# Kernel tuning notes

Measured on AMD Instinct MI355X. Metric: run time of the kernel, lower is better.

The kernel has to match this reference:

```python
import jax, jax.numpy as jnp
import numpy as np

N_NODES = 50000


def gcn_conv(x, W, b, src, dst, n):
    """PyG-style GCNConv: symmetric-normalized aggregation over A + I.
    x: [N, Fin], W: [Fin, Fout], b: [Fout], src/dst: [E] int edge endpoints.
    """
    h = x @ W  # [N, Fout]
    # degree with self-loops: deg[i] = 1 + in-degree(i)
    deg = jnp.zeros((n,), dtype=h.dtype).at[dst].add(1.0) + 1.0
    dinv = jax.lax.rsqrt(deg)  # deg^-1/2
    norm_e = dinv[src] * dinv[dst]  # [E]
    # message passing: sum_j norm_ij * h_j  (plus self-loop term deg_i^-1 * h_i)
    agg = jnp.zeros_like(h).at[dst].add(h[src] * norm_e[:, None])
    agg = agg + h * (dinv * dinv)[:, None]
    return agg + b


def setup_inputs() -> dict:
    key = jax.random.key(0)
    ks = jax.random.split(key, 9)
    N, F_in, H, C = N_NODES, 128, 64, 4
    E = 1600000
    node_features = jax.random.normal(ks[0], (N, F_in), dtype=jnp.float32)
    edge_index = jax.random.randint(ks[1], (2, E), 0, N, dtype=jnp.int32)
    s1 = 1.0 / np.sqrt(F_in)
    s2 = 1.0 / np.sqrt(H)
    W1 = jax.random.uniform(ks[2], (F_in, H), jnp.float32, -s1, s1)
    b1 = jax.random.uniform(ks[3], (H,), jnp.float32, -s1, s1)
    W2 = jax.random.uniform(ks[4], (H, H), jnp.float32, -s2, s2)
    b2 = jax.random.uniform(ks[5], (H,), jnp.float32, -s2, s2)
    W3 = jax.random.uniform(ks[6], (H, C), jnp.float32, -s2, s2)
    b3 = jax.random.uniform(ks[7], (C,), jnp.float32, -s2, s2)
    return {"node_features": node_features, "edge_index": edge_index,
            "W1": W1, "b1": b1, "W2": W2, "b2": b2, "W3": W3, "b3": b3}


def reference(node_features, edge_index, W1, b1, W2, b2, W3, b3):
    n = node_features.shape[0]
    src, dst = edge_index[0], edge_index[1]
    out = jax.nn.relu(gcn_conv(node_features, W1, b1, src, dst, n))
    # layer2 applied 7 times with SHARED weights (faithful to the source)
    for _ in range(7):
        out = jax.nn.relu(gcn_conv(out, W2, b2, src, dst, n))
    out = gcn_conv(out, W3, b3, src, dst, n)
    return jax.nn.softmax(out, axis=0)  # softmax over the node dimension (dim=0)
```

## Files before the change

kernel.cpp:

```cpp
#include <hip/hip_runtime.h>
#include <hip/hip_fp16.h>
#include <math.h>
#include <float.h>



__global__ __launch_bounds__(256) void k_count(const int* __restrict__ dst,
                                               unsigned* __restrict__ deg, int E) {
    int e = blockIdx.x * 256 + threadIdx.x;
    if (e < E) atomicAdd(&deg[dst[e]], 1u);
}

__global__ __launch_bounds__(256) void k_dinv(const unsigned* __restrict__ deg,
                                              float* __restrict__ dinv, int n) {
    int i = blockIdx.x * 256 + threadIdx.x;
    if (i < n) dinv[i] = rsqrtf(1.0f + (float)deg[i]);
}

__global__ __launch_bounds__(256) void k_scan1(const unsigned* __restrict__ deg,
                                               int* __restrict__ row_start,
                                               unsigned* __restrict__ bsum, int n) {
    __shared__ unsigned t[256];
    int i = blockIdx.x * 256 + threadIdx.x;
    unsigned v = (i < n) ? deg[i] : 0u;
    t[threadIdx.x] = v;
    __syncthreads();
    #pragma unroll
    for (int off = 1; off < 256; off <<= 1) {
        unsigned u = (threadIdx.x >= (unsigned)off) ? t[threadIdx.x - off] : 0u;
        __syncthreads();
        t[threadIdx.x] += u;
        __syncthreads();
    }
    if (i < n) row_start[i] = (int)(t[threadIdx.x] - v);
    if (threadIdx.x == 255) bsum[blockIdx.x] = t[255];
}

__global__ __launch_bounds__(256) void k_scan2(unsigned* __restrict__ bsum,
                                               int* __restrict__ row_start,
                                               int nb, int n) {
    __shared__ unsigned t[256];
    unsigned v = (threadIdx.x < (unsigned)nb) ? bsum[threadIdx.x] : 0u;
    t[threadIdx.x] = v;
    __syncthreads();
    #pragma unroll
    for (int off = 1; off < 256; off <<= 1) {
        unsigned u = (threadIdx.x >= (unsigned)off) ? t[threadIdx.x - off] : 0u;
        __syncthreads();
        t[threadIdx.x] += u;
        __syncthreads();
    }
    if (threadIdx.x < (unsigned)nb) bsum[threadIdx.x] = t[threadIdx.x] - v;
    if (threadIdx.x == 255) row_start[n] = (int)t[255];
}

__global__ __launch_bounds__(256) void k_scan3(int* __restrict__ row_start,
                                               const unsigned* __restrict__ bsum, int n) {
    int i = blockIdx.x * 256 + threadIdx.x;
    if (i < n) row_start[i] += (int)bsum[blockIdx.x];
}

__global__ __launch_bounds__(256) void k_fill(const int* __restrict__ src,
                                              const int* __restrict__ dst,
                                              const int* __restrict__ row_start,
                                              unsigned* __restrict__ cursor,
                                              int* __restrict__ csr_src, int E) {
    int e = blockIdx.x * 256 + threadIdx.x;
    if (e >= E) return;
    int s = src[e], d = dst[e];
    unsigned pos = atomicAdd(&cursor[d], 1u);
    csr_src[row_start[d] + (int)pos] = s;
}


__global__ __launch_bounds__(256) void k_gemm64_f32(const float* __restrict__ x,
                                                    const float* __restrict__ W,
                                                    const float* __restrict__ dinv,
                                                    __half* __restrict__ hs, int n) {
    __shared__ float Wl[128 * 64];
    for (int idx = threadIdx.x; idx < 128 * 64; idx += 256) Wl[idx] = W[idx];
    __syncthreads();
    int wave = threadIdx.x >> 6, lane = threadIdx.x & 63;
    int base = blockIdx.x * 64 + wave * 16;
    for (int it = 0; it < 16; ++it) {
        int i = base + it;
        if (i < n) {
            const float4* xr = (const float4*)(x + (size_t)i * 128);
            float acc = 0.f;
            #pragma unroll
            for (int k4 = 0; k4 < 32; ++k4) {
                float4 v = xr[k4];
                acc += v.x * Wl[(k4 * 4 + 0) * 64 + lane];
                acc += v.y * Wl[(k4 * 4 + 1) * 64 + lane];
                acc += v.z * Wl[(k4 * 4 + 2) * 64 + lane];
                acc += v.w * Wl[(k4 * 4 + 3) * 64 + lane];
            }
            hs[(size_t)i * 64 + lane] = __float2half(acc * dinv[i]);
        }
    }
}


__global__ __launch_bounds__(256) void k_gemm64_f16(const __half* __restrict__ xh,
                                                    const float* __restrict__ W,
                                                    const float* __restrict__ dinv,
                                                    __half* __restrict__ hs, int n) {
    __shared__ float Wl[64 * 64];
    for (int idx = threadIdx.x; idx < 64 * 64; idx += 256) Wl[idx] = W[idx];
    __syncthreads();
    int wave = threadIdx.x >> 6, lane = threadIdx.x & 63;
    int base = blockIdx.x * 64 + wave * 16;
    for (int it = 0; it < 16; ++it) {
        int i = base + it;
        if (i < n) {
            const __half2* xr = (const __half2*)(xh + (size_t)i * 64);
            float acc = 0.f;
            #pragma unroll
            for (int k2 = 0; k2 < 32; ++k2) {
                float2 v = __half22float2(xr[k2]);
                acc += v.x * Wl[(k2 * 2 + 0) * 64 + lane];
                acc += v.y * Wl[(k2 * 2 + 1) * 64 + lane];
            }
            hs[(size_t)i * 64 + lane] = __float2half(acc * dinv[i]);
        }
    }
}

__global__ __launch_bounds__(256) void k_gemm4(const __half* __restrict__ xh,
                                               const float* __restrict__ W,
                                               const float* __restrict__ dinv,
                                               float4* __restrict__ h4, int n) {
    __shared__ float Wl[256];
    for (int idx = threadIdx.x; idx < 256; idx += 256) Wl[idx] = W[idx];
    __syncthreads();
    int i = blockIdx.x * 256 + threadIdx.x;
    if (i >= n) return;
    const __half2* ar = (const __half2*)(xh + (size_t)i * 64);
    float a0 = 0.f, a1 = 0.f, a2 = 0.f, a3 = 0.f;
    #pragma unroll
    for (int k2 = 0; k2 < 32; ++k2) {
        float2 v = __half22float2(ar[k2]);
        int k = k2 * 2;
        a0 += v.x * Wl[k * 4 + 0] + v.y * Wl[(k + 1) * 4 + 0];
        a1 += v.x * Wl[k * 4 + 1] + v.y * Wl[(k + 1) * 4 + 1];
        a2 += v.x * Wl[k * 4 + 2] + v.y * Wl[(k + 1) * 4 + 2];
        a3 += v.x * Wl[k * 4 + 3] + v.y * Wl[(k + 1) * 4 + 3];
    }
    float di = dinv[i];
    h4[i] = make_float4(a0 * di, a1 * di, a2 * di, a3 * di);
}


__global__ __launch_bounds__(256) void k_agg64h(const __half* __restrict__ hs,
                                                const float* __restrict__ dinv,
                                                const int* __restrict__ row_start,
                                                const int* __restrict__ csr_src,
                                                const float* __restrict__ bias,
                                                __half* __restrict__ out, int n) {
    int gw = (int)((blockIdx.x * 256 + threadIdx.x) >> 6);
    int lane = threadIdx.x & 63;
    if (gw >= n) return;
    float acc = __half2float(hs[(size_t)gw * 64 + lane]);
    int s = row_start[gw], e = row_start[gw + 1];
    int slot = s;
    for (; slot + 8 <= e; slot += 8) {
        int i0 = csr_src[slot + 0], i1 = csr_src[slot + 1];
        int i2 = csr_src[slot + 2], i3 = csr_src[slot + 3];
        int i4 = csr_src[slot + 4], i5 = csr_src[slot + 5];
        int i6 = csr_src[slot + 6], i7 = csr_src[slot + 7];
        float v0 = __half2float(hs[(size_t)i0 * 64 + lane]);
        float v1 = __half2float(hs[(size_t)i1 * 64 + lane]);
        float v2 = __half2float(hs[(size_t)i2 * 64 + lane]);
        float v3 = __half2float(hs[(size_t)i3 * 64 + lane]);
        float v4 = __half2float(hs[(size_t)i4 * 64 + lane]);
        float v5 = __half2float(hs[(size_t)i5 * 64 + lane]);
        float v6 = __half2float(hs[(size_t)i6 * 64 + lane]);
        float v7 = __half2float(hs[(size_t)i7 * 64 + lane]);
        acc += ((v0 + v1) + (v2 + v3)) + ((v4 + v5) + (v6 + v7));
    }
    for (; slot < e; ++slot)
        acc += __half2float(hs[(size_t)csr_src[slot] * 64 + lane]);
    acc = acc * dinv[gw] + bias[lane];
    out[(size_t)gw * 64 + lane] = __float2half(fmaxf(acc, 0.f));
}


__global__ __launch_bounds__(256) void k_agg4(const float4* __restrict__ h4,
                                              const float* __restrict__ dinv,
                                              const int* __restrict__ row_start,
                                              const int* __restrict__ csr_src,
                                              const float* __restrict__ b3,
                                              float4* __restrict__ z, int n) {
    int i = blockIdx.x * 256 + threadIdx.x;
    if (i >= n) return;
    float4 self = h4[i];
    float a0 = self.x, a1 = self.y, a2 = self.z, a3 = self.w;
    int s = row_start[i], e = row_start[i + 1];
    int slot = s;
    for (; slot + 4 <= e; slot += 4) {
        int s0 = csr_src[slot], s1 = csr_src[slot + 1];
        int s2 = csr_src[slot + 2], s3 = csr_src[slot + 3];
        float4 v0 = h4[s0], v1 = h4[s1], v2 = h4[s2], v3 = h4[s3];
        a0 += v0.x + v1.x + v2.x + v3.x;
        a1 += v0.y + v1.y + v2.y + v3.y;
        a2 += v0.z + v1.z + v2.z + v3.z;
        a3 += v0.w + v1.w + v2.w + v3.w;
    }
    for (; slot < e; ++slot) {
        float4 v = h4[csr_src[slot]];
        a0 += v.x; a1 += v.y; a2 += v.z; a3 += v.w;
    }
    float di = dinv[i];
    z[i] = make_float4(a0 * di + b3[0], a1 * di + b3[1],
                       a2 * di + b3[2], a3 * di + b3[3]);
}


__device__ inline unsigned encf(float f) {
    unsigned u = __float_as_uint(f);
    return (u & 0x80000000u) ? ~u : (u | 0x80000000u);
}
__device__ inline float decf(unsigned e) {
    return (e & 0x80000000u) ? __uint_as_float(e & 0x7FFFFFFFu) : __uint_as_float(~e);
}

__global__ __launch_bounds__(256) void k_max(const float4* __restrict__ z,
                                             unsigned* __restrict__ gmax, int n) {
    float m0 = -FLT_MAX, m1 = -FLT_MAX, m2 = -FLT_MAX, m3 = -FLT_MAX;
    for (int i = blockIdx.x * 256 + threadIdx.x; i < n; i += gridDim.x * 256) {
        float4 v = z[i];
        m0 = fmaxf(m0, v.x); m1 = fmaxf(m1, v.y);
        m2 = fmaxf(m2, v.z); m3 = fmaxf(m3, v.w);
    }
    #pragma unroll
    for (int off = 32; off; off >>= 1) {
        m0 = fmaxf(m0, __shfl_xor(m0, off));
        m1 = fmaxf(m1, __shfl_xor(m1, off));
        m2 = fmaxf(m2, __shfl_xor(m2, off));
        m3 = fmaxf(m3, __shfl_xor(m3, off));
    }
    if ((threadIdx.x & 63) == 0) {
        atomicMax(&gmax[0], encf(m0));
        atomicMax(&gmax[1], encf(m1));
        atomicMax(&gmax[2], encf(m2));
        atomicMax(&gmax[3], encf(m3));
    }
}

__global__ __launch_bounds__(256) void k_exp(const float4* __restrict__ z,
                                             float4* __restrict__ out,
                                             const unsigned* __restrict__ gmax,
                                             float* __restrict__ gsum, int n) {
    float M0 = decf(gmax[0]), M1 = decf(gmax[1]), M2 = decf(gmax[2]), M3 = decf(gmax[3]);
    float s0 = 0.f, s1 = 0.f, s2 = 0.f, s3 = 0.f;
    for (int i = blockIdx.x * 256 + threadIdx.x; i < n; i += gridDim.x * 256) {
        float4 v = z[i];
        float4 e;
        e.x = expf(v.x - M0); e.y = expf(v.y - M1);
        e.z = expf(v.z - M2); e.w = expf(v.w - M3);
        out[i] = e;
        s0 += e.x; s1 += e.y; s2 += e.z; s3 += e.w;
    }
    #pragma unroll
    for (int off = 32; off; off >>= 1) {
        s0 += __shfl_xor(s0, off);
        s1 += __shfl_xor(s1, off);
        s2 += __shfl_xor(s2, off);
        s3 += __shfl_xor(s3, off);
    }
    if ((threadIdx.x & 63) == 0) {
        atomicAdd(&gsum[0], s0);
        atomicAdd(&gsum[1], s1);
        atomicAdd(&gsum[2], s2);
        atomicAdd(&gsum[3], s3);
    }
}

__global__ __launch_bounds__(256) void k_norm(float4* __restrict__ out,
                                              const float* __restrict__ gsum, int n) {
    float r0 = 1.f / gsum[0], r1 = 1.f / gsum[1], r2 = 1.f / gsum[2], r3 = 1.f / gsum[3];
    for (int i = blockIdx.x * 256 + threadIdx.x; i < n; i += gridDim.x * 256) {
        float4 v = out[i];
        v.x *= r0; v.y *= r1; v.z *= r2; v.w *= r3;
        out[i] = v;
    }
}


extern "C" void kernel_launch(void* const* d_in, const int* in_sizes, int n_in,
                              void* d_out, int out_size, void* d_ws, size_t ws_size,
                              hipStream_t stream) {
    const float* x0 = (const float*)d_in[0];
    const int* ei = (const int*)d_in[1];
    const float* W1 = (const float*)d_in[2];
    const float* b1 = (const float*)d_in[3];
    const float* W2 = (const float*)d_in[4];
    const float* b2 = (const float*)d_in[5];
    const float* W3 = (const float*)d_in[6];
    const float* b3 = (const float*)d_in[7];

    const int n = in_sizes[0] / 128;
    const int E = in_sizes[1] / 2;
    const int* src = ei;
    const int* dst = ei + E;

    char* ws = (char*)d_ws;
    size_t off = 0;
    auto alloc = [&](size_t bytes) -> void* {
        void* p = (void*)(ws + off);
        off = (off + bytes + 255) & ~(size_t)255;
        return p;
    };

    unsigned* deg    = (unsigned*)alloc((size_t)n * 4);
    unsigned* cursor = (unsigned*)alloc((size_t)n * 4);
    unsigned* gmax   = (unsigned*)alloc(16);
    float*    gsum   = (float*)alloc(16);
    size_t zero_bytes = off;

    float* dinv      = (float*)alloc((size_t)n * 4);
    int*   row_start = (int*)alloc((size_t)(n + 1) * 4);
    unsigned* bsum   = (unsigned*)alloc(1024 * 4);
    int*   csr_src   = (int*)alloc((size_t)E * 4);
    __half* hbuf     = (__half*)alloc((size_t)n * 64 * 2);
    __half* xbuf     = (__half*)alloc((size_t)n * 64 * 2);
    float4* h4buf    = (float4*)alloc((size_t)n * 16);
    float4* zbuf     = (float4*)alloc((size_t)n * 16);

    hipMemsetAsync(deg, 0, zero_bytes, stream);

    const int nbE = (E + 255) / 256;
    const int nbN = (n + 255) / 256;

    k_count<<<nbE, 256, 0, stream>>>(dst, deg, E);
    k_dinv<<<nbN, 256, 0, stream>>>(deg, dinv, n);
    k_scan1<<<nbN, 256, 0, stream>>>(deg, row_start, bsum, n);
    k_scan2<<<1, 256, 0, stream>>>(bsum, row_start, nbN, n);
    k_scan3<<<nbN, 256, 0, stream>>>(row_start, bsum, n);
    k_fill<<<nbE, 256, 0, stream>>>(src, dst, row_start, cursor, csr_src, E);

    const int nbG = (n + 63) / 64;
    const int nbA = (n * 64 + 255) / 256;

    k_gemm64_f32<<<nbG, 256, 0, stream>>>(x0, W1, dinv, hbuf, n);
    k_agg64h<<<nbA, 256, 0, stream>>>(hbuf, dinv, row_start, csr_src, b1, xbuf, n);

    for (int l = 0; l < 7; ++l) {
        k_gemm64_f16<<<nbG, 256, 0, stream>>>(xbuf, W2, dinv, hbuf, n);
        k_agg64h<<<nbA, 256, 0, stream>>>(hbuf, dinv, row_start, csr_src, b2, xbuf, n);
    }

    k_gemm4<<<nbN, 256, 0, stream>>>(xbuf, W3, dinv, h4buf, n);
    k_agg4<<<nbN, 256, 0, stream>>>(h4buf, dinv, row_start, csr_src, b3, zbuf, n);

    k_max<<<256, 256, 0, stream>>>(zbuf, gmax, n);
    k_exp<<<256, 256, 0, stream>>>(zbuf, (float4*)d_out, gmax, gsum, n);
    k_norm<<<256, 256, 0, stream>>>((float4*)d_out, gsum, n);
}
```

Before: 985.8 us.

## Partition CSR count/fill atomics by destination range and widen aggregation unroll

The degree-count and CSR-fill kernels now launch a fixed grid of 8 partitions times 104 blocks. Each block strides over all edges but only does atomics for destinations in its partition's node range, and blockIdx low bits pick the partition. The intent is to keep each partition's atomics in a narrower address range, likely to localise them per XCD/L2 and cut cross-die atomic traffic, at the cost of every partition re-reading the full dst array. Separately, the hidden-layer aggregation loop now gathers 16 neighbours per iteration instead of 8, with a 4-wide remainder loop, to get more memory loads in flight.

```diff
diff --git a/kernel.cpp b/kernel.cpp
--- a/kernel.cpp
+++ b/kernel.cpp
@@ -4,11 +4,20 @@
 #include <float.h>
 
 
+#define NPART 8
+#define BPP   104
+
 
 __global__ __launch_bounds__(256) void k_count(const int* __restrict__ dst,
-                                               unsigned* __restrict__ deg, int E) {
-    int e = blockIdx.x * 256 + threadIdx.x;
-    if (e < E) atomicAdd(&deg[dst[e]], 1u);
+                                               unsigned* __restrict__ deg,
+                                               int E, int chunk) {
+    int part = blockIdx.x & (NPART - 1);
+    int q = blockIdx.x >> 3;
+    int lo = part * chunk, hi = lo + chunk;
+    for (int e = q * 256 + threadIdx.x; e < E; e += 256 * BPP) {
+        int d = dst[e];
+        if (d >= lo && d < hi) atomicAdd(&deg[d], 1u);
+    }
 }
 
 __global__ __launch_bounds__(256) void k_dinv(const unsigned* __restrict__ deg,
@@ -64,12 +73,19 @@
                                               const int* __restrict__ dst,
                                               const int* __restrict__ row_start,
                                               unsigned* __restrict__ cursor,
-                                              int* __restrict__ csr_src, int E) {
-    int e = blockIdx.x * 256 + threadIdx.x;
-    if (e >= E) return;
-    int s = src[e], d = dst[e];
-    unsigned pos = atomicAdd(&cursor[d], 1u);
-    csr_src[row_start[d] + (int)pos] = s;
+                                              int* __restrict__ csr_src,
+                                              int E, int chunk) {
+    int part = blockIdx.x & (NPART - 1);
+    int q = blockIdx.x >> 3;
+    int lo = part * chunk, hi = lo + chunk;
+    for (int e = q * 256 + threadIdx.x; e < E; e += 256 * BPP) {
+        int d = dst[e];
+        if (d >= lo && d < hi) {
+            int s = src[e];
+            unsigned pos = atomicAdd(&cursor[d], 1u);
+            csr_src[row_start[d] + (int)pos] = s;
+        }
+    }
 }
 
 
@@ -163,20 +179,25 @@
     float acc = __half2float(hs[(size_t)gw * 64 + lane]);
     int s = row_start[gw], e = row_start[gw + 1];
     int slot = s;
-    for (; slot + 8 <= e; slot += 8) {
+    for (; slot + 16 <= e; slot += 16) {
+        int idx[16];
+        #pragma unroll
+        for (int j = 0; j < 16; ++j) idx[j] = csr_src[slot + j];
+        float v[16];
+        #pragma unroll
+        for (int j = 0; j < 16; ++j) v[j] = __half2float(hs[(size_t)idx[j] * 64 + lane]);
+        float t0 = ((v[0] + v[1]) + (v[2] + v[3])) + ((v[4] + v[5]) + (v[6] + v[7]));
+        float t1 = ((v[8] + v[9]) + (v[10] + v[11])) + ((v[12] + v[13]) + (v[14] + v[15]));
+        acc += t0 + t1;
+    }
+    for (; slot + 4 <= e; slot += 4) {
         int i0 = csr_src[slot + 0], i1 = csr_src[slot + 1];
         int i2 = csr_src[slot + 2], i3 = csr_src[slot + 3];
-        int i4 = csr_src[slot + 4], i5 = csr_src[slot + 5];
-        int i6 = csr_src[slot + 6], i7 = csr_src[slot + 7];
         float v0 = __half2float(hs[(size_t)i0 * 64 + lane]);
         float v1 = __half2float(hs[(size_t)i1 * 64 + lane]);
         float v2 = __half2float(hs[(size_t)i2 * 64 + lane]);
         float v3 = __half2float(hs[(size_t)i3 * 64 + lane]);
-        float v4 = __half2float(hs[(size_t)i4 * 64 + lane]);
-        float v5 = __half2float(hs[(size_t)i5 * 64 + lane]);
-        float v6 = __half2float(hs[(size_t)i6 * 64 + lane]);
-        float v7 = __half2float(hs[(size_t)i7 * 64 + lane]);
-        acc += ((v0 + v1) + (v2 + v3)) + ((v4 + v5) + (v6 + v7));
+        acc += (v0 + v1) + (v2 + v3);
     }
     for (; slot < e; ++slot)
         acc += __half2float(hs[(size_t)csr_src[slot] * 64 + lane]);
@@ -303,6 +324,7 @@
     const int E = in_sizes[1] / 2;
     const int* src = ei;
     const int* dst = ei + E;
+    const int chunk = (n + NPART - 1) / NPART;
 
     char* ws = (char*)d_ws;
     size_t off = 0;
@@ -329,15 +351,14 @@
 
     hipMemsetAsync(deg, 0, zero_bytes, stream);
 
-    const int nbE = (E + 255) / 256;
     const int nbN = (n + 255) / 256;
 
-    k_count<<<nbE, 256, 0, stream>>>(dst, deg, E);
+    k_count<<<NPART * BPP, 256, 0, stream>>>(dst, deg, E, chunk);
     k_dinv<<<nbN, 256, 0, stream>>>(deg, dinv, n);
     k_scan1<<<nbN, 256, 0, stream>>>(deg, row_start, bsum, n);
     k_scan2<<<1, 256, 0, stream>>>(bsum, row_start, nbN, n);
     k_scan3<<<nbN, 256, 0, stream>>>(row_start, bsum, n);
-    k_fill<<<nbE, 256, 0, stream>>>(src, dst, row_start, cursor, csr_src, E);
+    k_fill<<<NPART * BPP, 256, 0, stream>>>(src, dst, row_start, cursor, csr_src, E, chunk);
 
     const int nbG = (n + 63) / 64;
     const int nbA = (n * 64 + 255) / 256;
```

Result: faster. 899.4 us (-8.8%).
